# Performance work log

Hardware: AMD Instinct MI355X
Metric: run time of the kernel (lower is better)

## Reference

```python
import jax, jax.numpy as jnp
import numpy as np

N_NODES = 50000
N_REL = 16
D_EMB = 128
D_HID = 128
D_OUT = 128
N_EDGES = 1600000


def _xavier(key, shape, fan_in, fan_out, dtype=jnp.float32):
    lim = float(np.sqrt(6.0 / (fan_in + fan_out)))
    return jax.random.uniform(key, shape, dtype, -lim, lim)


def setup_inputs() -> dict:
    key = jax.random.key(0)
    ks = jax.random.split(key, 10)
    edge_index = jax.random.randint(ks[0], (2, N_EDGES), 0, N_NODES, dtype=jnp.int64)
    edge_type = jax.random.randint(ks[1], (N_EDGES,), 0, N_REL, dtype=jnp.int64)
    emb = _xavier(ks[2], (N_NODES, D_EMB), N_NODES, D_EMB)
    W1 = _xavier(ks[3], (N_REL, D_EMB, D_HID), D_EMB, D_HID)
    root1 = _xavier(ks[4], (D_EMB, D_HID), D_EMB, D_HID)
    b1 = jnp.zeros((D_HID,), jnp.float32)
    W2 = _xavier(ks[5], (N_REL, D_HID, D_OUT), D_HID, D_OUT)
    root2 = _xavier(ks[6], (D_HID, D_OUT), D_HID, D_OUT)
    b2 = jnp.zeros((D_OUT,), jnp.float32)
    return {"edge_index": edge_index, "edge_type": edge_type, "emb": emb,
            "W1": W1, "root1": root1, "b1": b1,
            "W2": W2, "root2": root2, "b2": b2}


def rgcn_conv(x, edge_index, edge_type, W, W_root, b):
    """PyG RGCNConv (num_bases=None): out_i = x_i @ W_root + b + sum_r mean_{j in N_r(i)} x_j @ W_r.
    Mean-aggregate x_j per (dst, relation) first, then apply relation GEMMs (linearity)."""
    src, dst = edge_index[0], edge_index[1]
    seg = dst * N_REL + edge_type                      # [E] composite (node, rel) key
    x_src = x[src]                                     # [E, d] gather
    summed = jax.ops.segment_sum(x_src, seg, num_segments=N_NODES * N_REL)  # [N*R, d]
    cnt = jax.ops.segment_sum(jnp.ones((src.shape[0],), x.dtype), seg,
                              num_segments=N_NODES * N_REL)                 # [N*R]
    agg = summed / jnp.maximum(cnt, 1.0)[:, None]      # mean; empty (i,r) -> 0
    agg = agg.reshape(N_NODES, N_REL, x.shape[1])      # [N, R, d]
    return jnp.einsum('nrd,rdh->nh', agg, W) + x @ W_root + b


def reference(edge_index, edge_type, emb, W1, root1, b1, W2, root2, b2):
    x = emb                                            # embedding.weight: all-node lookup
    x = jax.nn.relu(rgcn_conv(x, edge_index, edge_type, W1, root1, b1))
    # dropout(p=0.5) omitted: eval-mode identity
    x = rgcn_conv(x, edge_index, edge_type, W2, root2, b2)
    return x
```

## Files before the change

kernel.cpp:

```cpp
#include <hip/hip_runtime.h>

#define N_NODES 50000
#define N_REL 16
#define D 128
#define N_SEG (N_NODES * N_REL)

typedef short bf16x8 __attribute__((ext_vector_type(8)));
typedef float f32x4 __attribute__((ext_vector_type(4)));
typedef unsigned short u16;
typedef unsigned int u32;

__device__ __forceinline__ u16 f32_to_bf16(float f) {
  u32 u = __builtin_bit_cast(u32, f);
  u32 r = (u + 0x7FFFu + ((u >> 16) & 1u)) >> 16;
  return (u16)r;
}
__device__ __forceinline__ float bf16_to_f32(u16 h) {
  u32 u = ((u32)h) << 16;
  return __builtin_bit_cast(float, u);
}

__global__ __launch_bounds__(256) void k_zero4(uint4* __restrict__ p, long long n4) {
  long long i = (long long)blockIdx.x * blockDim.x + threadIdx.x;
  long long stride = (long long)gridDim.x * blockDim.x;
  uint4 z; z.x = z.y = z.z = z.w = 0u;
  for (; i < n4; i += stride) p[i] = z;
}

__global__ __launch_bounds__(256) void k_count(const int* __restrict__ dst,
                                               const int* __restrict__ rel,
                                               int* __restrict__ cnt, int E) {
  int e = blockIdx.x * blockDim.x + threadIdx.x;
  if (e < E) atomicAdd(&cnt[dst[e] * N_REL + rel[e]], 1);
}

__global__ __launch_bounds__(256) void k_bsum(const int* __restrict__ cnt,
                                              int* __restrict__ bsum, int n) {
  __shared__ int sm[256];
  int i = blockIdx.x * 256 + threadIdx.x;
  int v = (i < n) ? cnt[i] : 0;
  sm[threadIdx.x] = v;
  __syncthreads();
  for (int s = 128; s > 0; s >>= 1) {
    if (threadIdx.x < s) sm[threadIdx.x] += sm[threadIdx.x + s];
    __syncthreads();
  }
  if (threadIdx.x == 0) bsum[blockIdx.x] = sm[0];
}

__global__ __launch_bounds__(1024) void k_bscan(int* __restrict__ bsum, int nb) {
  __shared__ int sm[1024];
  __shared__ int carry;
  if (threadIdx.x == 0) carry = 0;
  __syncthreads();
  int niter = (nb + 1023) / 1024;
  for (int it = 0; it < niter; ++it) {
    int i = it * 1024 + threadIdx.x;
    int v = (i < nb) ? bsum[i] : 0;
    sm[threadIdx.x] = v;
    __syncthreads();
    for (int s = 1; s < 1024; s <<= 1) {
      int t = (threadIdx.x >= s) ? sm[threadIdx.x - s] : 0;
      __syncthreads();
      sm[threadIdx.x] += t;
      __syncthreads();
    }
    int incl = sm[threadIdx.x];
    int c = carry;
    __syncthreads();
    if (i < nb) bsum[i] = c + incl - v;
    if (threadIdx.x == 1023) carry = c + sm[1023];
    __syncthreads();
  }
}

__global__ __launch_bounds__(256) void k_off(const int* __restrict__ cnt,
                                             const int* __restrict__ bsum,
                                             int* __restrict__ off, int n) {
  __shared__ int sm[256];
  int i = blockIdx.x * 256 + threadIdx.x;
  int v = (i < n) ? cnt[i] : 0;
  sm[threadIdx.x] = v;
  __syncthreads();
  for (int s = 1; s < 256; s <<= 1) {
    int t = (threadIdx.x >= s) ? sm[threadIdx.x - s] : 0;
    __syncthreads();
    sm[threadIdx.x] += t;
    __syncthreads();
  }
  int excl = sm[threadIdx.x] - v + bsum[blockIdx.x];
  if (i < n) off[i] = excl;
  if (i == n - 1) off[n] = excl + v;
}

__global__ __launch_bounds__(256) void k_fill(const int* __restrict__ src,
                                              const int* __restrict__ dst,
                                              const int* __restrict__ rel,
                                              const int* __restrict__ off,
                                              int* __restrict__ cnt,
                                              int* __restrict__ bucket, int E) {
  int e = blockIdx.x * blockDim.x + threadIdx.x;
  if (e >= E) return;
  int seg = dst[e] * N_REL + rel[e];
  int old = atomicSub(&cnt[seg], 1);
  bucket[off[seg] + old - 1] = src[e];
}

__device__ __forceinline__ void wfrag_one(const float* __restrict__ W,
                                          u16* __restrict__ Wf, int tid) {
  int lane = tid & 63;
  int t = (tid >> 6) & 7;
  int kb = tid >> 9;
  int h = t * 16 + (lane & 15);
  int kbase = kb * 32 + ((lane >> 4) << 3);
  bf16x8 frag;
#pragma unroll
  for (int j = 0; j < 8; ++j) {
    int k = kbase + j;
    frag[j] = (short)f32_to_bf16(W[(size_t)(k >> 7) * (D * D) + (size_t)(k & 127) * D + h]);
  }
  *(bf16x8*)(Wf + (size_t)tid * 8) = frag;
}

#define CVT_N4 (N_NODES * D / 4)
#define WF_T (64 * 8 * 64)
#define RF_T (4 * 8 * 64)
#define PREP_TOTAL (CVT_N4 + 2 * WF_T + 2 * RF_T)

__global__ __launch_bounds__(256) void k_prep(const float* __restrict__ emb,
                                              u16* __restrict__ embb,
                                              const float* __restrict__ W1,
                                              u16* __restrict__ Wf1,
                                              const float* __restrict__ W2,
                                              u16* __restrict__ Wf2,
                                              const float* __restrict__ R1,
                                              u16* __restrict__ Rf1,
                                              const float* __restrict__ R2,
                                              u16* __restrict__ Rf2) {
  int tid = blockIdx.x * blockDim.x + threadIdx.x;
  if (tid < CVT_N4) {
    float4 v = ((const float4*)emb)[tid];
    u32 p0 = (u32)f32_to_bf16(v.x) | ((u32)f32_to_bf16(v.y) << 16);
    u32 p1 = (u32)f32_to_bf16(v.z) | ((u32)f32_to_bf16(v.w) << 16);
    ((u32*)embb)[tid * 2] = p0;
    ((u32*)embb)[tid * 2 + 1] = p1;
    return;
  }
  int u = tid - CVT_N4;
  if (u < WF_T) { wfrag_one(W1, Wf1, u); return; }
  u -= WF_T;
  if (u < WF_T) { wfrag_one(W2, Wf2, u); return; }
  u -= WF_T;
  if (u < RF_T) { wfrag_one(R1, Rf1, u); return; }
  u -= RF_T;
  if (u < RF_T) { wfrag_one(R2, Rf2, u); return; }
}

template <int L>
__global__ __launch_bounds__(256) void k_layer(const int* __restrict__ off,
                                               const int* __restrict__ bucket,
                                               const u16* __restrict__ x,
                                               const u16* __restrict__ Wf,
                                               const u16* __restrict__ Rf,
                                               const float* __restrict__ bias,
                                               u16* __restrict__ outb,
                                               float* __restrict__ outf) {
  __shared__ f32x4 red[4][4][64];
  int w = threadIdx.x >> 6;
  int lane = threadIdx.x & 63;
  int node0 = blockIdx.x << 4;
  int m = lane & 15;
  int q = lane >> 4;
  int node = node0 + m;

  f32x4 acc[8];
#pragma unroll
  for (int t = 0; t < 8; ++t)
#pragma unroll
    for (int i = 0; i < 4; ++i) acc[t][i] = 0.0f;

  {
    bf16x8 a = *(const bf16x8*)(x + ((size_t)node << 7) + w * 32 + (q << 3));
    const u16* bp = Rf + ((size_t)w << 12) + ((size_t)lane << 3);
#pragma unroll
    for (int t = 0; t < 8; ++t) {
      bf16x8 b = *(const bf16x8*)(bp + t * 512);
      acc[t] = __builtin_amdgcn_mfma_f32_16x16x32_bf16(a, b, acc[t], 0, 0, 0);
    }
  }

  for (int rr = 0; rr < 4; ++rr) {
    int r = (w << 2) + rr;
    int seg = (node << 4) + r;
    int o0 = off[seg];
    int o1 = off[seg + 1];

    float a0[8], a1[8], a2[8], a3[8];
#pragma unroll
    for (int j = 0; j < 8; ++j) { a0[j] = 0.f; a1[j] = 0.f; a2[j] = 0.f; a3[j] = 0.f; }

    int i = o0;
    int s = (i < o1) ? bucket[i] : 0;
    while (i < o1) {
      const u16* xs = x + ((size_t)s << 7) + (q << 3);
      bf16x8 v0 = *(const bf16x8*)(xs);
      bf16x8 v1 = *(const bf16x8*)(xs + 32);
      bf16x8 v2 = *(const bf16x8*)(xs + 64);
      bf16x8 v3 = *(const bf16x8*)(xs + 96);
      int snext = (i + 1 < o1) ? bucket[i + 1] : 0;
#pragma unroll
      for (int j = 0; j < 8; ++j) {
        a0[j] += bf16_to_f32((u16)v0[j]);
        a1[j] += bf16_to_f32((u16)v1[j]);
        a2[j] += bf16_to_f32((u16)v2[j]);
        a3[j] += bf16_to_f32((u16)v3[j]);
      }
      s = snext;
      ++i;
    }

    float sc = (o1 > o0) ? 1.0f / (float)(o1 - o0) : 0.0f;
    bf16x8 f0, f1, f2, f3;
#pragma unroll
    for (int j = 0; j < 8; ++j) {
      f0[j] = (short)f32_to_bf16(a0[j] * sc);
      f1[j] = (short)f32_to_bf16(a1[j] * sc);
      f2[j] = (short)f32_to_bf16(a2[j] * sc);
      f3[j] = (short)f32_to_bf16(a3[j] * sc);
    }

    const u16* bp = Wf + ((size_t)(r * 4) << 12) + ((size_t)lane << 3);
#pragma unroll
    for (int t = 0; t < 8; ++t) {
      bf16x8 b0 = *(const bf16x8*)(bp + t * 512);
      bf16x8 b1 = *(const bf16x8*)(bp + 4096 + t * 512);
      bf16x8 b2 = *(const bf16x8*)(bp + 8192 + t * 512);
      bf16x8 b3 = *(const bf16x8*)(bp + 12288 + t * 512);
      acc[t] = __builtin_amdgcn_mfma_f32_16x16x32_bf16(f0, b0, acc[t], 0, 0, 0);
      acc[t] = __builtin_amdgcn_mfma_f32_16x16x32_bf16(f1, b1, acc[t], 0, 0, 0);
      acc[t] = __builtin_amdgcn_mfma_f32_16x16x32_bf16(f2, b2, acc[t], 0, 0, 0);
      acc[t] = __builtin_amdgcn_mfma_f32_16x16x32_bf16(f3, b3, acc[t], 0, 0, 0);
    }
  }

#pragma unroll
  for (int half = 0; half < 2; ++half) {
#pragma unroll
    for (int t = 0; t < 4; ++t) red[w][t][lane] = acc[half * 4 + t];
    __syncthreads();
    {
      f32x4 s0 = red[0][w][lane];
      f32x4 s1 = red[1][w][lane];
      f32x4 s2 = red[2][w][lane];
      f32x4 s3 = red[3][w][lane];
      int tt = half * 4 + w;
      int h = tt * 16 + m;
      float bv = bias[h];
#pragma unroll
      for (int r4 = 0; r4 < 4; ++r4) {
        int n = node0 + (q << 2) + r4;
        float v = s0[r4] + s1[r4] + s2[r4] + s3[r4] + bv;
        if (L == 1) {
          v = v > 0.0f ? v : 0.0f;
          outb[(size_t)n * D + h] = f32_to_bf16(v);
        } else {
          outf[(size_t)n * D + h] = v;
        }
      }
    }
    if (half == 0) __syncthreads();
  }
}

extern "C" void kernel_launch(void* const* d_in, const int* in_sizes, int n_in,
                              void* d_out, int out_size, void* d_ws, size_t ws_size,
                              hipStream_t stream) {
  const int* edge_index = (const int*)d_in[0];
  const int* edge_type  = (const int*)d_in[1];
  const float* emb   = (const float*)d_in[2];
  const float* W1    = (const float*)d_in[3];
  const float* root1 = (const float*)d_in[4];
  const float* b1    = (const float*)d_in[5];
  const float* W2    = (const float*)d_in[6];
  const float* root2 = (const float*)d_in[7];
  const float* b2    = (const float*)d_in[8];
  float* out = (float*)d_out;

  int E = in_sizes[0] / 2;
  const int* src = edge_index;
  const int* dst = edge_index + E;
  int nblocks_seg = (N_SEG + 255) / 256;

  char* ws = (char*)d_ws;
  size_t off_b = 0;
  auto take = [&](size_t bytes) -> char* {
    char* p = ws + off_b;
    off_b += (bytes + 255) & ~(size_t)255;
    return p;
  };
  int*   cnt    = (int*)take((size_t)N_SEG * 4);
  int*   offs   = (int*)take((size_t)(N_SEG + 1) * 4);
  int*   bsum   = (int*)take((size_t)nblocks_seg * 4);
  int*   bucket = (int*)take((size_t)E * 4);
  u16*   embb   = (u16*)take((size_t)N_NODES * D * 2);
  u16*   x1     = (u16*)take((size_t)N_NODES * D * 2);
  u16*   Wf1    = (u16*)take((size_t)64 * 8 * 512 * 2);
  u16*   Rf1    = (u16*)take((size_t)4 * 8 * 512 * 2);
  u16*   Wf2    = (u16*)take((size_t)64 * 8 * 512 * 2);
  u16*   Rf2    = (u16*)take((size_t)4 * 8 * 512 * 2);

  int eBlocks = (E + 255) / 256;
  int layerBlocks = N_NODES / 16;

  k_zero4<<<512, 256, 0, stream>>>((uint4*)cnt, (long long)N_SEG * 4 / 16);
  k_count<<<eBlocks, 256, 0, stream>>>(dst, edge_type, cnt, E);
  k_bsum<<<nblocks_seg, 256, 0, stream>>>(cnt, bsum, N_SEG);
  k_bscan<<<1, 1024, 0, stream>>>(bsum, nblocks_seg);
  k_off<<<nblocks_seg, 256, 0, stream>>>(cnt, bsum, offs, N_SEG);
  k_fill<<<eBlocks, 256, 0, stream>>>(src, dst, edge_type, offs, cnt, bucket, E);

  k_prep<<<(PREP_TOTAL + 255) / 256, 256, 0, stream>>>(emb, embb, W1, Wf1, W2, Wf2,
                                                       root1, Rf1, root2, Rf2);

  k_layer<1><<<layerBlocks, 256, 0, stream>>>(offs, bucket, embb, Wf1, Rf1, b1,
                                              x1, nullptr);
  k_layer<2><<<layerBlocks, 256, 0, stream>>>(offs, bucket, x1, Wf2, Rf2, b2,
                                              nullptr, out);
}
```

Measured before the change: 521.2 us.

## Split relations across eight waves per block instead of four

Each layer block now runs 512 threads (8 waves), and each wave handles 2 relations instead of 4. The root GEMM runs only on waves 0-3, and the cross-wave reduction through shared memory sums 8 partial accumulators. The segment offsets are loaded up front as three consecutive values. The aim is more memory-level parallelism in the latency-bound gather loop. In exchange, shared memory per block doubles, the reduction adds work, and the 512-thread launch bound may cap registers per thread.

After: 528.6 us. About the same (+1.4%).

```diff
diff --git a/kernel.cpp b/kernel.cpp
--- a/kernel.cpp
+++ b/kernel.cpp
@@ -157,7 +157,7 @@
 }
 
 template <int L>
-__global__ __launch_bounds__(256) void k_layer(const int* __restrict__ off,
+__global__ __launch_bounds__(512) void k_layer(const int* __restrict__ off,
                                                const int* __restrict__ bucket,
                                                const u16* __restrict__ x,
                                                const u16* __restrict__ Wf,
@@ -165,7 +165,7 @@
                                                const float* __restrict__ bias,
                                                u16* __restrict__ outb,
                                                float* __restrict__ outf) {
-  __shared__ f32x4 red[4][4][64];
+  __shared__ f32x4 red[8][4][64];
   int w = threadIdx.x >> 6;
   int lane = threadIdx.x & 63;
   int node0 = blockIdx.x << 4;
@@ -179,7 +179,12 @@
 #pragma unroll
     for (int i = 0; i < 4; ++i) acc[t][i] = 0.0f;
 
-  {
+  int segb = (node << 4) + (w << 1);
+  int o_0 = off[segb];
+  int o_1 = off[segb + 1];
+  int o_2 = off[segb + 2];
+
+  if (w < 4) {
     bf16x8 a = *(const bf16x8*)(x + ((size_t)node << 7) + w * 32 + (q << 3));
     const u16* bp = Rf + ((size_t)w << 12) + ((size_t)lane << 3);
 #pragma unroll
@@ -189,25 +194,20 @@
     }
   }
 
-  for (int rr = 0; rr < 4; ++rr) {
-    int r = (w << 2) + rr;
-    int seg = (node << 4) + r;
-    int o0 = off[seg];
-    int o1 = off[seg + 1];
-
+  auto do_rel = [&](int r, int lo, int hi) {
     float a0[8], a1[8], a2[8], a3[8];
 #pragma unroll
     for (int j = 0; j < 8; ++j) { a0[j] = 0.f; a1[j] = 0.f; a2[j] = 0.f; a3[j] = 0.f; }
 
-    int i = o0;
-    int s = (i < o1) ? bucket[i] : 0;
-    while (i < o1) {
+    int i = lo;
+    int s = (i < hi) ? bucket[i] : 0;
+    while (i < hi) {
       const u16* xs = x + ((size_t)s << 7) + (q << 3);
       bf16x8 v0 = *(const bf16x8*)(xs);
       bf16x8 v1 = *(const bf16x8*)(xs + 32);
       bf16x8 v2 = *(const bf16x8*)(xs + 64);
       bf16x8 v3 = *(const bf16x8*)(xs + 96);
-      int snext = (i + 1 < o1) ? bucket[i + 1] : 0;
+      int snext = (i + 1 < hi) ? bucket[i + 1] : 0;
 #pragma unroll
       for (int j = 0; j < 8; ++j) {
         a0[j] += bf16_to_f32((u16)v0[j]);
@@ -219,7 +219,7 @@
       ++i;
     }
 
-    float sc = (o1 > o0) ? 1.0f / (float)(o1 - o0) : 0.0f;
+    float sc = (hi > lo) ? 1.0f / (float)(hi - lo) : 0.0f;
     bf16x8 f0, f1, f2, f3;
 #pragma unroll
     for (int j = 0; j < 8; ++j) {
@@ -241,25 +241,34 @@
       acc[t] = __builtin_amdgcn_mfma_f32_16x16x32_bf16(f2, b2, acc[t], 0, 0, 0);
       acc[t] = __builtin_amdgcn_mfma_f32_16x16x32_bf16(f3, b3, acc[t], 0, 0, 0);
     }
-  }
+  };
+
+  int rbase = w << 1;
+  do_rel(rbase + 0, o_0, o_1);
+  do_rel(rbase + 1, o_1, o_2);
 
 #pragma unroll
   for (int half = 0; half < 2; ++half) {
 #pragma unroll
     for (int t = 0; t < 4; ++t) red[w][t][lane] = acc[half * 4 + t];
     __syncthreads();
-    {
+    if (w < 4) {
       f32x4 s0 = red[0][w][lane];
       f32x4 s1 = red[1][w][lane];
       f32x4 s2 = red[2][w][lane];
       f32x4 s3 = red[3][w][lane];
+      f32x4 s4 = red[4][w][lane];
+      f32x4 s5 = red[5][w][lane];
+      f32x4 s6 = red[6][w][lane];
+      f32x4 s7 = red[7][w][lane];
       int tt = half * 4 + w;
       int h = tt * 16 + m;
       float bv = bias[h];
 #pragma unroll
       for (int r4 = 0; r4 < 4; ++r4) {
         int n = node0 + (q << 2) + r4;
-        float v = s0[r4] + s1[r4] + s2[r4] + s3[r4] + bv;
+        float v = s0[r4] + s1[r4] + s2[r4] + s3[r4] +
+                  s4[r4] + s5[r4] + s6[r4] + s7[r4] + bv;
         if (L == 1) {
           v = v > 0.0f ? v : 0.0f;
           outb[(size_t)n * D + h] = f32_to_bf16(v);
@@ -322,8 +331,8 @@
   k_prep<<<(PREP_TOTAL + 255) / 256, 256, 0, stream>>>(emb, embb, W1, Wf1, W2, Wf2,
                                                        root1, Rf1, root2, Rf2);
 
-  k_layer<1><<<layerBlocks, 256, 0, stream>>>(offs, bucket, embb, Wf1, Rf1, b1,
+  k_layer<1><<<layerBlocks, 512, 0, stream>>>(offs, bucket, embb, Wf1, Rf1, b1,
                                               x1, nullptr);
-  k_layer<2><<<layerBlocks, 256, 0, stream>>>(offs, bucket, x1, Wf2, Rf2, b2,
+  k_layer<2><<<layerBlocks, 512, 0, stream>>>(offs, bucket, x1, Wf2, Rf2, b2,
                                               nullptr, out);
 }
```
